# Kernel optimization log

Measured on AMD Instinct MI355X. Metric: run time of the kernel, lower is better.

Reference implementation:

```python
import jax, jax.numpy as jnp
import numpy as np
import math

B, LT, LS, D, H, DFF = 4, 1024, 1024, 1024, 16, 4096
DK = D // H
EPS = 1e-5


def setup_inputs() -> dict:
    key = jax.random.key(0)
    ks = jax.random.split(key, 32)
    n = lambda i, shape, s=0.02: jax.random.normal(ks[i], shape, jnp.float32) * s
    inp = {
        'tgt': jax.random.normal(ks[0], (B, LT, D), jnp.float32),
        'memory': jax.random.normal(ks[1], (B, LS, D), jnp.float32),
        'src_pad_mask': jnp.zeros((B, LT, LS), dtype=bool),
        'tgt_mask': jnp.broadcast_to(jnp.triu(jnp.ones((LT, LT), dtype=bool), 1), (B, LT, LT)),
        # self-attention projections
        'self_wq': n(2, (D, D)), 'self_bq': jnp.zeros((D,)),
        'self_wk': n(3, (D, D)), 'self_bk': jnp.zeros((D,)),
        'self_wv': n(4, (D, D)), 'self_bv': jnp.zeros((D,)),
        'self_wo': n(5, (D, D)), 'self_bo': jnp.zeros((D,)),
        # cross-attention projections
        'cross_wq': n(6, (D, D)), 'cross_bq': jnp.zeros((D,)),
        'cross_wk': n(7, (D, D)), 'cross_bk': jnp.zeros((D,)),
        'cross_wv': n(8, (D, D)), 'cross_bv': jnp.zeros((D,)),
        'cross_wo': n(9, (D, D)), 'cross_bo': jnp.zeros((D,)),
        # layer norms (pre-norm)
        'ln1_g': jnp.ones((D,)), 'ln1_b': jnp.zeros((D,)),
        'ln2_g': jnp.ones((D,)), 'ln2_b': jnp.zeros((D,)),
        'ln3_g': jnp.ones((D,)), 'ln3_b': jnp.zeros((D,)),
        # feed forward
        'ffn_w1': n(10, (D, DFF)), 'ffn_b1': jnp.zeros((DFF,)),
        'ffn_w2': n(11, (DFF, D)), 'ffn_b2': jnp.zeros((D,)),
    }
    return inp


def _layernorm(x, g, b):
    mu = jnp.mean(x, axis=-1, keepdims=True)
    var = jnp.mean(jnp.square(x - mu), axis=-1, keepdims=True)
    return (x - mu) * jax.lax.rsqrt(var + EPS) * g + b


def _mha(xq, xkv, wq, bq, wk, bk, wv, bv, wo, bo, mask):
    b, lq, d = xq.shape
    lk = xkv.shape[1]
    q = (xq @ wq + bq).reshape(b, lq, H, DK).transpose(0, 2, 1, 3) / math.sqrt(DK)
    k = (xkv @ wk + bk).reshape(b, lk, H, DK).transpose(0, 2, 1, 3)
    v = (xkv @ wv + bv).reshape(b, lk, H, DK).transpose(0, 2, 1, 3)
    scores = jnp.einsum('bhqd,bhkd->bhqk', q, k)  # [B,H,Lq,Lk]
    scores = jnp.where(mask[:, None], -1e18, scores)
    attn = jax.nn.softmax(scores, axis=-1)  # dropout p=0 (eval)
    ctx = jnp.einsum('bhqk,bhkd->bhqd', attn, v)
    ctx = ctx.transpose(0, 2, 1, 3).reshape(b, lq, d)
    return ctx @ wo + bo


def reference(tgt, memory, src_pad_mask, tgt_mask,
              self_wq, self_bq, self_wk, self_bk, self_wv, self_bv, self_wo, self_bo,
              cross_wq, cross_bq, cross_wk, cross_bk, cross_wv, cross_bv, cross_wo, cross_bo,
              ln1_g, ln1_b, ln2_g, ln2_b, ln3_g, ln3_b,
              ffn_w1, ffn_b1, ffn_w2, ffn_b2):
    # pre-norm sublayer 1: self attention
    x = tgt + _mha(_layernorm(tgt, ln1_g, ln1_b), _layernorm(tgt, ln1_g, ln1_b),
                   self_wq, self_bq, self_wk, self_bk, self_wv, self_bv, self_wo, self_bo, tgt_mask)
    # pre-norm sublayer 2: cross attention
    x = x + _mha(_layernorm(x, ln2_g, ln2_b), memory,
                 cross_wq, cross_bq, cross_wk, cross_bk, cross_wv, cross_bv, cross_wo, cross_bo, src_pad_mask)
    # pre-norm sublayer 3: FFN
    h = _layernorm(x, ln3_g, ln3_b)
    x = x + (jax.nn.gelu(h @ ffn_w1 + ffn_b1) @ ffn_w2 + ffn_b2)
    return x
```

## Files before the change

kernel.cpp:

```cpp
#include <hip/hip_runtime.h>

typedef unsigned short u16;
typedef __attribute__((ext_vector_type(8))) __bf16 bf16x8;
typedef __attribute__((ext_vector_type(4))) float floatx4;

__device__ inline float bf2f(u16 u) {
    union { unsigned int i; float f; } x; x.i = ((unsigned int)u) << 16; return x.f;
}
__device__ inline u16 f2bf(float f) {
    __bf16 h = (__bf16)f; return __builtin_bit_cast(unsigned short, h);
}
__device__ inline float load_f(u16 v) { return bf2f(v); }
__device__ inline float load_f(float v) { return v; }

__device__ inline floatx4 mfma_bf16(bf16x8 a, bf16x8 b, floatx4 c) {
    return __builtin_amdgcn_mfma_f32_16x16x32_bf16(a, b, c, 0, 0, 0);
}

__device__ inline float gelu_tanh(float x) {
    float u = 0.7978845608028654f * (x + 0.044715f * x * x * x);
    u = fminf(fmaxf(u, -15.f), 15.f);
    float e = __expf(2.f * u);
    float th = (e - 1.f) / (e + 1.f);
    return 0.5f * x * (1.f + th);
}

__device__ inline void async16(const void* g, void* l) {
    __builtin_amdgcn_global_load_lds(
        (const __attribute__((address_space(1))) unsigned int*)g,
        (__attribute__((address_space(3))) unsigned int*)l, 16, 0, 0);
}

__global__ __launch_bounds__(256)
void detect_dtype(const u16* __restrict__ p, int* __restrict__ flag) {
    int t = threadIdx.x, cnt = 0;
    #pragma unroll
    for (int j = 0; j < 8; ++j) {
        unsigned e = (p[t * 8 + j] >> 7) & 0xFF;
        cnt += (e >= 100 && e <= 140) ? 1 : 0;
    }
    __shared__ int s[256];
    s[t] = cnt; __syncthreads();
    for (int off = 128; off; off >>= 1) { if (t < off) s[t] += s[t + off]; __syncthreads(); }
    if (t == 0) *flag = (s[0] < 1844) ? 1 : 0;
}

__global__ __launch_bounds__(256)
void convert_to_bf16(const void* __restrict__ src, u16* __restrict__ dst, int n,
                     const int* __restrict__ flag) {
    int f = *flag;
    int i = (blockIdx.x * 256 + threadIdx.x) * 4;
    if (i < n) {
        #pragma unroll
        for (int j = 0; j < 4; ++j)
            dst[i + j] = f ? f2bf(((const float*)src)[i + j]) : ((const u16*)src)[i + j];
    }
}

__global__ __launch_bounds__(256)
void convert_tgt(const void* __restrict__ src, u16* __restrict__ dst,
                 float* __restrict__ X, int n, const int* __restrict__ flag) {
    int f = *flag;
    int i = (blockIdx.x * 256 + threadIdx.x) * 4;
    if (i < n) {
        #pragma unroll
        for (int j = 0; j < 4; ++j) {
            float v; u16 hv;
            if (f) { v = ((const float*)src)[i + j]; hv = f2bf(v); }
            else   { hv = ((const u16*)src)[i + j]; v = bf2f(hv); }
            dst[i + j] = hv;
            X[i + j] = v;
        }
    }
}

struct VecTab { const void* src[16]; int n[16]; int off[16]; };
__global__ __launch_bounds__(256)
void convert_vecs(VecTab tab, u16* __restrict__ dst, const int* __restrict__ flag) {
    int f = *flag;
    int b = blockIdx.x;
    const void* s = tab.src[b];
    int n = tab.n[b];
    u16* d = dst + tab.off[b];
    for (int i = threadIdx.x; i < n; i += 256)
        d[i] = f ? f2bf(((const float*)s)[i]) : ((const u16*)s)[i];
}

__global__ __launch_bounds__(256)
void store_out(const float* __restrict__ X, void* __restrict__ out, int n,
               const int* __restrict__ flag) {
    int f = *flag;
    int i = (blockIdx.x * 256 + threadIdx.x) * 4;
    if (i < n) {
        #pragma unroll
        for (int j = 0; j < 4; ++j) {
            float v = X[i + j];
            if (f) ((float*)out)[i + j] = v;
            else   ((u16*)out)[i + j] = f2bf(v);
        }
    }
}

__global__ __launch_bounds__(256)
void transpose_any(const void* __restrict__ src, u16* __restrict__ dst, int R, int C,
                   const int* __restrict__ flag) {
    int f = *flag;
    __shared__ u16 tile[32][33];
    int tx = threadIdx.x & 31, ty = threadIdx.x >> 5;
    int r0 = blockIdx.y * 32, c0 = blockIdx.x * 32;
    #pragma unroll
    for (int i = 0; i < 32; i += 8) {
        size_t idx = (size_t)(r0 + ty + i) * C + c0 + tx;
        tile[ty + i][tx] = f ? f2bf(((const float*)src)[idx]) : ((const u16*)src)[idx];
    }
    __syncthreads();
    #pragma unroll
    for (int i = 0; i < 32; i += 8)
        dst[(size_t)(c0 + ty + i) * R + r0 + tx] = tile[tx][ty + i];
}

template <typename TIN>
__global__ __launch_bounds__(256)
void lnorm(const TIN* __restrict__ Xin, const u16* __restrict__ gg,
           const u16* __restrict__ bb, u16* __restrict__ Y) {
    const int row = blockIdx.x, t = threadIdx.x;
    const TIN* xr = Xin + (size_t)row * 1024;
    float x[4]; float s1 = 0.f, s2 = 0.f;
    #pragma unroll
    for (int i = 0; i < 4; ++i) {
        float v = load_f(xr[i * 256 + t]);
        x[i] = v; s1 += v; s2 += v * v;
    }
    #pragma unroll
    for (int m = 1; m < 64; m <<= 1) { s1 += __shfl_xor(s1, m, 64); s2 += __shfl_xor(s2, m, 64); }
    __shared__ float red[8];
    if ((t & 63) == 0) { red[(t >> 6) * 2] = s1; red[(t >> 6) * 2 + 1] = s2; }
    __syncthreads();
    s1 = red[0] + red[2] + red[4] + red[6];
    s2 = red[1] + red[3] + red[5] + red[7];
    float mu = s1 * (1.f / 1024.f);
    float var = s2 * (1.f / 1024.f) - mu * mu;
    float rs = rsqrtf(var + 1e-5f);
    #pragma unroll
    for (int i = 0; i < 4; ++i) {
        int idx = i * 256 + t;
        float yv = (x[i] - mu) * rs * bf2f(gg[idx]) + bf2f(bb[idx]);
        Y[(size_t)row * 1024 + idx] = f2bf(yv);
    }
}

__global__ __launch_bounds__(256, 2)
void gemm_bt2(const u16* __restrict__ A, const u16* __restrict__ Bt,
              const u16* __restrict__ bias, u16* __restrict__ C,
              float* __restrict__ Xres, int M, int N, int K, int ldc, int epi) {
    __shared__ alignas(16) u16 As[128 * 32];
    __shared__ alignas(16) u16 Bs[128 * 32];
    const int t = threadIdx.x;
    const int lane = t & 63, w = t >> 6;
    const int l15 = lane & 15, quad = lane >> 4;
    const int m0 = blockIdx.y * 128, n0 = blockIdx.x * 128;
    const int wm = (w >> 1) * 64, wn = (w & 1) * 64;
    const int ksl = K / gridDim.z;
    const int kb = blockIdx.z * ksl, ke = kb + ksl;
    const int srow = lane >> 2, scol = (lane & 3) * 8;
    const u16* ga = A + (size_t)(m0 + w * 32 + srow) * K + scol;
    const u16* gb = Bt + (size_t)(n0 + w * 32 + srow) * K + scol;
    u16* lA0 = &As[(w * 32) * 32];
    u16* lA1 = &As[(w * 32 + 16) * 32];
    u16* lB0 = &Bs[(w * 32) * 32];
    u16* lB1 = &Bs[(w * 32 + 16) * 32];
    floatx4 acc[4][4] = {};

    for (int k0 = kb; k0 < ke; k0 += 32) {
        __syncthreads();
        async16(ga + k0, lA0);
        async16(ga + (size_t)16 * K + k0, lA1);
        async16(gb + k0, lB0);
        async16(gb + (size_t)16 * K + k0, lB1);
        __syncthreads();
        bf16x8 af[4], bfr[4];
        #pragma unroll
        for (int i = 0; i < 4; ++i) {
            af[i]  = *(const bf16x8*)&As[(wm + i * 16 + l15) * 32 + quad * 8];
            bfr[i] = *(const bf16x8*)&Bs[(wn + i * 16 + l15) * 32 + quad * 8];
        }
        #pragma unroll
        for (int mi = 0; mi < 4; ++mi)
            #pragma unroll
            for (int ni = 0; ni < 4; ++ni)
                acc[mi][ni] = mfma_bf16(af[mi], bfr[ni], acc[mi][ni]);
    }

    const bool addb = (blockIdx.z == 0);
    #pragma unroll
    for (int mi = 0; mi < 4; ++mi) {
        #pragma unroll
        for (int ni = 0; ni < 4; ++ni) {
            int gn = n0 + wn + ni * 16 + l15;
            float bv = addb ? bf2f(bias[gn]) : 0.f;
            #pragma unroll
            for (int r = 0; r < 4; ++r) {
                int gm = m0 + wm + mi * 16 + quad * 4 + r;
                float v = acc[mi][ni][r] + bv;
                size_t idx = (size_t)gm * ldc + gn;
                if (epi == 0)      C[idx] = f2bf(v);
                else if (epi == 1) C[idx] = f2bf(gelu_tanh(v));
                else               atomicAdd(&Xres[idx], v);
            }
        }
    }
}

#define SCL2 0.18033688011112042f
__global__ __launch_bounds__(256, 2)
void attn_fwd2(const u16* __restrict__ QKV, u16* __restrict__ CTX, int causal) {
    __shared__ alignas(16) u16 Ks[64 * 72];
    __shared__ alignas(16) u16 Vst[64 * 72];
    __shared__ alignas(16) u16 Sw[4][16 * 72];
    const int t = threadIdx.x;
    const int lane = t & 63, w = t >> 6;
    const int l15 = lane & 15, quad = lane >> 4;
    const int q0 = blockIdx.x * 64, h = blockIdx.y, b = blockIdx.z;
    const int qrow = q0 + w * 16 + l15;
    const u16* qp = QKV + (size_t)(b * 1024 + qrow) * 3072 + h * 64;
    bf16x8 aq0 = *(const bf16x8*)(qp + quad * 8);
    bf16x8 aq1 = *(const bf16x8*)(qp + 32 + quad * 8);
    floatx4 O[4] = {};
    float mo[4], lo[4];
    #pragma unroll
    for (int r = 0; r < 4; ++r) { mo[r] = -1e30f; lo[r] = 0.f; }

    const int skey = t >> 2, snn = t & 3, sd0 = (t & 3) * 16;
    const int swz = skey ^ (snn << 3);
    const int kend = causal ? (q0 + 64) : 1024;
    for (int kt = 0; kt < kend; kt += 64) {
        __syncthreads();
        {
            const u16* kvb = QKV + (size_t)(b * 1024 + kt + skey) * 3072 + h * 64 + sd0;
            bf16x8 k0v = *(const bf16x8*)(kvb + 1024);
            bf16x8 k1v = *(const bf16x8*)(kvb + 1024 + 8);
            *(bf16x8*)&Ks[skey * 72 + sd0] = k0v;
            *(bf16x8*)&Ks[skey * 72 + sd0 + 8] = k1v;
            bf16x8 v0v = *(const bf16x8*)(kvb + 2048);
            bf16x8 v1v = *(const bf16x8*)(kvb + 2048 + 8);
            #pragma unroll
            for (int j = 0; j < 8; ++j) Vst[(sd0 + j) * 72 + swz] = ((u16*)&v0v)[j];
            #pragma unroll
            for (int j = 0; j < 8; ++j) Vst[(sd0 + 8 + j) * 72 + swz] = ((u16*)&v1v)[j];
        }
        __syncthreads();
        floatx4 S[4];
        #pragma unroll
        for (int kg = 0; kg < 4; ++kg) {
            bf16x8 bk0 = *(const bf16x8*)&Ks[(kg * 16 + l15) * 72 + quad * 8];
            bf16x8 bk1 = *(const bf16x8*)&Ks[(kg * 16 + l15) * 72 + 32 + quad * 8];
            floatx4 z = {};
            z = mfma_bf16(aq0, bk0, z);
            z = mfma_bf16(aq1, bk1, z);
            S[kg] = z;
        }
        const bool domask = causal && (kt == q0);
        float al[4];
        #pragma unroll
        for (int r = 0; r < 4; ++r) {
            #pragma unroll
            for (int kg = 0; kg < 4; ++kg) {
                float s = S[kg][r] * SCL2;
                if (domask) {
                    int kg_glob = kt + kg * 16 + l15;
                    int qg = q0 + w * 16 + quad * 4 + r;
                    if (kg_glob > qg) s = -1e30f;
                }
                S[kg][r] = s;
            }
            float v = fmaxf(fmaxf(S[0][r], S[1][r]), fmaxf(S[2][r], S[3][r]));
            #pragma unroll
            for (int msk = 1; msk < 16; msk <<= 1) v = fmaxf(v, __shfl_xor(v, msk, 64));
            float mn = fmaxf(mo[r], v);
            al[r] = exp2f(mo[r] - mn);
            float ssum = 0.f;
            #pragma unroll
            for (int kg = 0; kg < 4; ++kg) {
                float p = exp2f(S[kg][r] - mn);
                S[kg][r] = p; ssum += p;
            }
            #pragma unroll
            for (int msk = 1; msk < 16; msk <<= 1) ssum += __shfl_xor(ssum, msk, 64);
            lo[r] = lo[r] * al[r] + ssum;
            mo[r] = mn;
        }
        #pragma unroll
        for (int kg = 0; kg < 4; ++kg)
            #pragma unroll
            for (int r = 0; r < 4; ++r)
                Sw[w][(quad * 4 + r) * 72 + kg * 16 + l15] = f2bf(S[kg][r]);
        #pragma unroll
        for (int g = 0; g < 4; ++g)
            #pragma unroll
            for (int r = 0; r < 4; ++r)
                O[g][r] *= al[r];
        bf16x8 ap0 = *(const bf16x8*)&Sw[w][l15 * 72 + quad * 8];
        bf16x8 ap1 = *(const bf16x8*)&Sw[w][l15 * 72 + 32 + quad * 8];
        #pragma unroll
        for (int g = 0; g < 4; ++g) {
            bf16x8 bv0 = *(const bf16x8*)&Vst[(g * 16 + l15) * 72 + ((quad ^ g) << 3)];
            bf16x8 bv1 = *(const bf16x8*)&Vst[(g * 16 + l15) * 72 + 32 + ((quad ^ g) << 3)];
            O[g] = mfma_bf16(ap0, bv0, O[g]);
            O[g] = mfma_bf16(ap1, bv1, O[g]);
        }
    }
    #pragma unroll
    for (int r = 0; r < 4; ++r) {
        float inv = 1.0f / lo[r];
        int qg = q0 + w * 16 + quad * 4 + r;
        #pragma unroll
        for (int g = 0; g < 4; ++g)
            CTX[(size_t)(b * 1024 + qg) * 1024 + h * 64 + g * 16 + l15] = f2bf(O[g][r] * inv);
    }
}

extern "C" void kernel_launch(void* const* d_in, const int* in_sizes, int n_in,
                              void* d_out, int out_size, void* d_ws, size_t ws_size,
                              hipStream_t stream) {
    const void* tgt_raw    = d_in[0];
    const void* memory_raw = d_in[1];

    char* ws = (char*)d_ws;
    const size_t MiB = 1024 * 1024;
    float* X   = (float*)ws;
    u16* Y     = (u16*)(ws + 16 * MiB);
    u16* QKV   = (u16*)(ws + 24 * MiB);
    u16* CTX   = (u16*)(ws + 48 * MiB);
    u16* H1    = (u16*)(ws + 24 * MiB);
    u16* wt    = (u16*)(ws + 56 * MiB);
    u16* wqkv_s = wt;
    u16* wo_s  = wt + 3 * 1048576;
    u16* wq_c  = wt + 4 * 1048576;
    u16* wkv_c = wt + 5 * 1048576;
    u16* wo_c  = wt + 7 * 1048576;
    u16* w1t   = wt + 8 * 1048576;
    u16* w2t   = wt + 12 * 1048576;
    u16* tgt_c = (u16*)(ws + 88 * MiB);
    u16* mem_c = (u16*)(ws + 96 * MiB);
    u16* vecs  = (u16*)(ws + 104 * MiB);
    int* flag  = (int*)(ws + 105 * MiB);

    dim3 blk(256);
    detect_dtype<<<1, blk, 0, stream>>>((const u16*)tgt_raw, flag);
    convert_tgt<<<4096, blk, 0, stream>>>(tgt_raw, tgt_c, X, 4096 * 1024, flag);
    convert_to_bf16<<<4096, blk, 0, stream>>>(memory_raw, mem_c, 4096 * 1024, flag);

    VecTab tab;
    const int srcIdx[16] = {5, 7, 9, 11, 13, 15, 17, 19, 20, 21, 22, 23, 24, 25, 27, 29};
    const int offs[16]   = {0, 1024, 2048, 3072, 4096, 5120, 6144, 7168,
                            8192, 9216, 10240, 11264, 12288, 13312, 14336, 18432};
    for (int i = 0; i < 16; ++i) {
        tab.src[i] = d_in[srcIdx[i]];
        tab.n[i] = (i == 14) ? 4096 : 1024;
        tab.off[i] = offs[i];
    }
    convert_vecs<<<16, blk, 0, stream>>>(tab, vecs, flag);
    u16* b_qkv_s = vecs;            u16* b_o_s  = vecs + 3072;
    u16* b_q_c   = vecs + 4096;     u16* b_kv_c = vecs + 5120;
    u16* b_o_c   = vecs + 7168;
    u16* g1 = vecs + 8192;  u16* be1 = vecs + 9216;
    u16* g2 = vecs + 10240; u16* be2 = vecs + 11264;
    u16* g3 = vecs + 12288; u16* be3 = vecs + 13312;
    u16* b_ff1 = vecs + 14336; u16* b_ff2 = vecs + 18432;

    dim3 tg32(32, 32);
    transpose_any<<<tg32, blk, 0, stream>>>(d_in[4],  wqkv_s,               1024, 1024, flag);
    transpose_any<<<tg32, blk, 0, stream>>>(d_in[6],  wqkv_s + 1048576,     1024, 1024, flag);
    transpose_any<<<tg32, blk, 0, stream>>>(d_in[8],  wqkv_s + 2 * 1048576, 1024, 1024, flag);
    transpose_any<<<tg32, blk, 0, stream>>>(d_in[10], wo_s,                 1024, 1024, flag);
    transpose_any<<<tg32, blk, 0, stream>>>(d_in[12], wq_c,                 1024, 1024, flag);
    transpose_any<<<tg32, blk, 0, stream>>>(d_in[14], wkv_c,                1024, 1024, flag);
    transpose_any<<<tg32, blk, 0, stream>>>(d_in[16], wkv_c + 1048576,      1024, 1024, flag);
    transpose_any<<<tg32, blk, 0, stream>>>(d_in[18], wo_c,                 1024, 1024, flag);
    transpose_any<<<dim3(128, 32), blk, 0, stream>>>(d_in[26], w1t, 1024, 4096, flag);
    transpose_any<<<dim3(32, 128), blk, 0, stream>>>(d_in[28], w2t, 4096, 1024, flag);

    const int NTOK = 4096;
    dim3 g1k(8, 32), g2k(16, 32), g3k(24, 32), g4k(32, 32);
    dim3 g1k_s2(8, 32, 2);
    dim3 g1k_s4(8, 32, 4);
    dim3 ga(16, 16, 4);

    lnorm<u16><<<4096, blk, 0, stream>>>(tgt_c, g1, be1, Y);
    gemm_bt2<<<g3k, blk, 0, stream>>>(Y, wqkv_s, b_qkv_s, QKV, nullptr, NTOK, 3072, 1024, 3072, 0);
    attn_fwd2<<<ga, blk, 0, stream>>>(QKV, CTX, 1);
    gemm_bt2<<<g1k_s2, blk, 0, stream>>>(CTX, wo_s, b_o_s, nullptr, X, NTOK, 1024, 1024, 1024, 2);

    lnorm<float><<<4096, blk, 0, stream>>>(X, g2, be2, Y);
    gemm_bt2<<<g1k, blk, 0, stream>>>(Y, wq_c, b_q_c, QKV, nullptr, NTOK, 1024, 1024, 3072, 0);
    gemm_bt2<<<g2k, blk, 0, stream>>>(mem_c, wkv_c, b_kv_c, QKV + 1024, nullptr, NTOK, 2048, 1024, 3072, 0);
    attn_fwd2<<<ga, blk, 0, stream>>>(QKV, CTX, 0);
    gemm_bt2<<<g1k_s2, blk, 0, stream>>>(CTX, wo_c, b_o_c, nullptr, X, NTOK, 1024, 1024, 1024, 2);

    lnorm<float><<<4096, blk, 0, stream>>>(X, g3, be3, Y);
    gemm_bt2<<<g4k, blk, 0, stream>>>(Y, w1t, b_ff1, H1, nullptr, NTOK, 4096, 1024, 4096, 1);
    gemm_bt2<<<g1k_s4, blk, 0, stream>>>(H1, w2t, b_ff2, nullptr, X, NTOK, 1024, 4096, 1024, 2);

    store_out<<<4096, blk, 0, stream>>>(X, d_out, NTOK * 1024, flag);
}
```

Baseline: 738.9 us.

## Batch transposes and conversions, template GEMM tile height, drop split-K atomics

Merges the ten weight transposes into one table-driven launch and the two input conversions into one kernel, which cuts launch overhead. Templates the GEMM on M-tile height and uses 64-row tiles without split-K for the N=1024 GEMMs, so the residual add becomes a plain read-modify-write instead of atomics. FFN2 keeps a 2-way split with atomics. Occupancy hints rise to 4 blocks per CU for GEMM and attention, which may raise register pressure or cause spills.

```diff
diff --git a/kernel.cpp b/kernel.cpp
--- a/kernel.cpp
+++ b/kernel.cpp
@@ -46,31 +46,22 @@
 }
 
 __global__ __launch_bounds__(256)
-void convert_to_bf16(const void* __restrict__ src, u16* __restrict__ dst, int n,
-                     const int* __restrict__ flag) {
+void convert_big(const void* __restrict__ tgt, const void* __restrict__ mem,
+                 u16* __restrict__ tgt_c, u16* __restrict__ mem_c,
+                 float* __restrict__ X, const int* __restrict__ flag) {
     int f = *flag;
-    int i = (blockIdx.x * 256 + threadIdx.x) * 4;
-    if (i < n) {
-        #pragma unroll
-        for (int j = 0; j < 4; ++j)
-            dst[i + j] = f ? f2bf(((const float*)src)[i + j]) : ((const u16*)src)[i + j];
-    }
-}
-
-__global__ __launch_bounds__(256)
-void convert_tgt(const void* __restrict__ src, u16* __restrict__ dst,
-                 float* __restrict__ X, int n, const int* __restrict__ flag) {
-    int f = *flag;
-    int i = (blockIdx.x * 256 + threadIdx.x) * 4;
-    if (i < n) {
-        #pragma unroll
-        for (int j = 0; j < 4; ++j) {
-            float v; u16 hv;
-            if (f) { v = ((const float*)src)[i + j]; hv = f2bf(v); }
-            else   { hv = ((const u16*)src)[i + j]; v = bf2f(hv); }
-            dst[i + j] = hv;
-            X[i + j] = v;
-        }
+    int b = blockIdx.x;
+    bool isT = b < 4096;
+    const void* s = isT ? tgt : mem;
+    u16* d = isT ? tgt_c : mem_c;
+    int i = (((isT ? b : b - 4096) * 256) + threadIdx.x) * 4;
+    #pragma unroll
+    for (int j = 0; j < 4; ++j) {
+        float v; u16 hv;
+        if (f) { v = ((const float*)s)[i + j]; hv = f2bf(v); }
+        else   { hv = ((const u16*)s)[i + j]; v = bf2f(hv); }
+        d[i + j] = hv;
+        if (isT) X[i + j] = v;
     }
 }
 
@@ -101,13 +92,27 @@
     }
 }
 
-__global__ __launch_bounds__(256)
-void transpose_any(const void* __restrict__ src, u16* __restrict__ dst, int R, int C,
-                   const int* __restrict__ flag) {
+struct TransTab {
+    const void* src[10]; u16* dst[10];
+    int C[10]; int start[10];
+};
+__global__ __launch_bounds__(256)
+void transpose_batch(TransTab tb, const int* __restrict__ flag) {
     int f = *flag;
+    int bid = blockIdx.x;
+    int seg = 0;
+    #pragma unroll
+    for (int i = 1; i < 10; ++i) if (bid >= tb.start[i]) seg = i;
+    int local = bid - tb.start[seg];
+    const void* src = tb.src[seg];
+    u16* dst = tb.dst[seg];
+    int C = tb.C[seg];
+    int ct = C >> 5;
+    int by = local / ct, bx = local - by * ct;
+    int R = (seg < 8) ? 1024 : ((seg == 8) ? 1024 : 4096);
     __shared__ u16 tile[32][33];
     int tx = threadIdx.x & 31, ty = threadIdx.x >> 5;
-    int r0 = blockIdx.y * 32, c0 = blockIdx.x * 32;
+    int r0 = by * 32, c0 = bx * 32;
     #pragma unroll
     for (int i = 0; i < 32; i += 8) {
         size_t idx = (size_t)(r0 + ty + i) * C + c0 + tx;
@@ -149,43 +154,47 @@
     }
 }
 
-__global__ __launch_bounds__(256, 2)
+template <int TM>
+__global__ __launch_bounds__(256, 4)
 void gemm_bt2(const u16* __restrict__ A, const u16* __restrict__ Bt,
               const u16* __restrict__ bias, u16* __restrict__ C,
               float* __restrict__ Xres, int M, int N, int K, int ldc, int epi) {
-    __shared__ alignas(16) u16 As[128 * 32];
+    __shared__ alignas(16) u16 As[TM * 32];
     __shared__ alignas(16) u16 Bs[128 * 32];
+    constexpr int MI = TM / 32;
+    constexpr int AROWS = TM / 4;
     const int t = threadIdx.x;
     const int lane = t & 63, w = t >> 6;
     const int l15 = lane & 15, quad = lane >> 4;
-    const int m0 = blockIdx.y * 128, n0 = blockIdx.x * 128;
-    const int wm = (w >> 1) * 64, wn = (w & 1) * 64;
+    const int m0 = blockIdx.y * TM, n0 = blockIdx.x * 128;
+    const int wm = (w >> 1) * (TM / 2), wn = (w & 1) * 64;
     const int ksl = K / gridDim.z;
     const int kb = blockIdx.z * ksl, ke = kb + ksl;
     const int srow = lane >> 2, scol = (lane & 3) * 8;
-    const u16* ga = A + (size_t)(m0 + w * 32 + srow) * K + scol;
+    const u16* ga = A + (size_t)(m0 + w * AROWS + srow) * K + scol;
     const u16* gb = Bt + (size_t)(n0 + w * 32 + srow) * K + scol;
-    u16* lA0 = &As[(w * 32) * 32];
-    u16* lA1 = &As[(w * 32 + 16) * 32];
+    u16* lA = &As[(w * AROWS) * 32];
     u16* lB0 = &Bs[(w * 32) * 32];
     u16* lB1 = &Bs[(w * 32 + 16) * 32];
-    floatx4 acc[4][4] = {};
+    floatx4 acc[MI][4] = {};
 
     for (int k0 = kb; k0 < ke; k0 += 32) {
         __syncthreads();
-        async16(ga + k0, lA0);
-        async16(ga + (size_t)16 * K + k0, lA1);
+        #pragma unroll
+        for (int c = 0; c < TM / 64; ++c)
+            async16(ga + (size_t)(c * 16) * K + k0, lA + c * 16 * 32);
         async16(gb + k0, lB0);
         async16(gb + (size_t)16 * K + k0, lB1);
         __syncthreads();
-        bf16x8 af[4], bfr[4];
-        #pragma unroll
-        for (int i = 0; i < 4; ++i) {
-            af[i]  = *(const bf16x8*)&As[(wm + i * 16 + l15) * 32 + quad * 8];
+        bf16x8 af[MI], bfr[4];
+        #pragma unroll
+        for (int i = 0; i < MI; ++i)
+            af[i] = *(const bf16x8*)&As[(wm + i * 16 + l15) * 32 + quad * 8];
+        #pragma unroll
+        for (int i = 0; i < 4; ++i)
             bfr[i] = *(const bf16x8*)&Bs[(wn + i * 16 + l15) * 32 + quad * 8];
-        }
-        #pragma unroll
-        for (int mi = 0; mi < 4; ++mi)
+        #pragma unroll
+        for (int mi = 0; mi < MI; ++mi)
             #pragma unroll
             for (int ni = 0; ni < 4; ++ni)
                 acc[mi][ni] = mfma_bf16(af[mi], bfr[ni], acc[mi][ni]);
@@ -193,7 +202,7 @@
 
     const bool addb = (blockIdx.z == 0);
     #pragma unroll
-    for (int mi = 0; mi < 4; ++mi) {
+    for (int mi = 0; mi < MI; ++mi) {
         #pragma unroll
         for (int ni = 0; ni < 4; ++ni) {
             int gn = n0 + wn + ni * 16 + l15;
@@ -205,6 +214,7 @@
                 size_t idx = (size_t)gm * ldc + gn;
                 if (epi == 0)      C[idx] = f2bf(v);
                 else if (epi == 1) C[idx] = f2bf(gelu_tanh(v));
+                else if (epi == 2) Xres[idx] += v;
                 else               atomicAdd(&Xres[idx], v);
             }
         }
@@ -212,7 +222,7 @@
 }
 
 #define SCL2 0.18033688011112042f
-__global__ __launch_bounds__(256, 2)
+__global__ __launch_bounds__(256, 4)
 void attn_fwd2(const u16* __restrict__ QKV, u16* __restrict__ CTX, int causal) {
     __shared__ alignas(16) u16 Ks[64 * 72];
     __shared__ alignas(16) u16 Vst[64 * 72];
@@ -347,8 +357,7 @@
 
     dim3 blk(256);
     detect_dtype<<<1, blk, 0, stream>>>((const u16*)tgt_raw, flag);
-    convert_tgt<<<4096, blk, 0, stream>>>(tgt_raw, tgt_c, X, 4096 * 1024, flag);
-    convert_to_bf16<<<4096, blk, 0, stream>>>(memory_raw, mem_c, 4096 * 1024, flag);
+    convert_big<<<8192, blk, 0, stream>>>(tgt_raw, memory_raw, tgt_c, mem_c, X, flag);
 
     VecTab tab;
     const int srcIdx[16] = {5, 7, 9, 11, 13, 15, 17, 19, 20, 21, 22, 23, 24, 25, 27, 29};
@@ -368,38 +377,41 @@
     u16* g3 = vecs + 12288; u16* be3 = vecs + 13312;
     u16* b_ff1 = vecs + 14336; u16* b_ff2 = vecs + 18432;
 
-    dim3 tg32(32, 32);
-    transpose_any<<<tg32, blk, 0, stream>>>(d_in[4],  wqkv_s,               1024, 1024, flag);
-    transpose_any<<<tg32, blk, 0, stream>>>(d_in[6],  wqkv_s + 1048576,     1024, 1024, flag);
-    transpose_any<<<tg32, blk, 0, stream>>>(d_in[8],  wqkv_s + 2 * 1048576, 1024, 1024, flag);
-    transpose_any<<<tg32, blk, 0, stream>>>(d_in[10], wo_s,                 1024, 1024, flag);
-    transpose_any<<<tg32, blk, 0, stream>>>(d_in[12], wq_c,                 1024, 1024, flag);
-    transpose_any<<<tg32, blk, 0, stream>>>(d_in[14], wkv_c,                1024, 1024, flag);
-    transpose_any<<<tg32, blk, 0, stream>>>(d_in[16], wkv_c + 1048576,      1024, 1024, flag);
-    transpose_any<<<tg32, blk, 0, stream>>>(d_in[18], wo_c,                 1024, 1024, flag);
-    transpose_any<<<dim3(128, 32), blk, 0, stream>>>(d_in[26], w1t, 1024, 4096, flag);
-    transpose_any<<<dim3(32, 128), blk, 0, stream>>>(d_in[28], w2t, 4096, 1024, flag);
+    TransTab tt;
+    const void* tsrc[10] = {d_in[4], d_in[6], d_in[8], d_in[10], d_in[12],
+                            d_in[14], d_in[16], d_in[18], d_in[26], d_in[28]};
+    u16* tdst[10] = {wqkv_s, wqkv_s + 1048576, wqkv_s + 2 * 1048576, wo_s, wq_c,
+                     wkv_c, wkv_c + 1048576, wo_c, w1t, w2t};
+    int start = 0;
+    for (int i = 0; i < 10; ++i) {
+        tt.src[i] = tsrc[i]; tt.dst[i] = tdst[i];
+        tt.C[i] = (i == 8) ? 4096 : 1024;
+        tt.start[i] = start;
+        int R = (i == 9) ? 4096 : 1024;
+        start += (R / 32) * (tt.C[i] / 32);
+    }
+    transpose_batch<<<start, blk, 0, stream>>>(tt, flag);
 
     const int NTOK = 4096;
-    dim3 g1k(8, 32), g2k(16, 32), g3k(24, 32), g4k(32, 32);
-    dim3 g1k_s2(8, 32, 2);
-    dim3 g1k_s4(8, 32, 4);
+    dim3 gQKV(24, 32), gKV(16, 32), gFF1(32, 32);
+    dim3 gN1k(8, 64);
+    dim3 gFF2(8, 64, 2);
     dim3 ga(16, 16, 4);
 
     lnorm<u16><<<4096, blk, 0, stream>>>(tgt_c, g1, be1, Y);
-    gemm_bt2<<<g3k, blk, 0, stream>>>(Y, wqkv_s, b_qkv_s, QKV, nullptr, NTOK, 3072, 1024, 3072, 0);
+    gemm_bt2<128><<<gQKV, blk, 0, stream>>>(Y, wqkv_s, b_qkv_s, QKV, nullptr, NTOK, 3072, 1024, 3072, 0);
     attn_fwd2<<<ga, blk, 0, stream>>>(QKV, CTX, 1);
-    gemm_bt2<<<g1k_s2, blk, 0, stream>>>(CTX, wo_s, b_o_s, nullptr, X, NTOK, 1024, 1024, 1024, 2);
+    gemm_bt2<64><<<gN1k, blk, 0, stream>>>(CTX, wo_s, b_o_s, nullptr, X, NTOK, 1024, 1024, 1024, 2);
 
     lnorm<float><<<4096, blk, 0, stream>>>(X, g2, be2, Y);
-    gemm_bt2<<<g1k, blk, 0, stream>>>(Y, wq_c, b_q_c, QKV, nullptr, NTOK, 1024, 1024, 3072, 0);
-    gemm_bt2<<<g2k, blk, 0, stream>>>(mem_c, wkv_c, b_kv_c, QKV + 1024, nullptr, NTOK, 2048, 1024, 3072, 0);
+    gemm_bt2<64><<<gN1k, blk, 0, stream>>>(Y, wq_c, b_q_c, QKV, nullptr, NTOK, 1024, 1024, 3072, 0);
+    gemm_bt2<128><<<gKV, blk, 0, stream>>>(mem_c, wkv_c, b_kv_c, QKV + 1024, nullptr, NTOK, 2048, 1024, 3072, 0);
     attn_fwd2<<<ga, blk, 0, stream>>>(QKV, CTX, 0);
-    gemm_bt2<<<g1k_s2, blk, 0, stream>>>(CTX, wo_c, b_o_c, nullptr, X, NTOK, 1024, 1024, 1024, 2);
+    gemm_bt2<64><<<gN1k, blk, 0, stream>>>(CTX, wo_c, b_o_c, nullptr, X, NTOK, 1024, 1024, 1024, 2);
 
     lnorm<float><<<4096, blk, 0, stream>>>(X, g3, be3, Y);
-    gemm_bt2<<<g4k, blk, 0, stream>>>(Y, w1t, b_ff1, H1, nullptr, NTOK, 4096, 1024, 4096, 1);
-    gemm_bt2<<<g1k_s4, blk, 0, stream>>>(H1, w2t, b_ff2, nullptr, X, NTOK, 1024, 4096, 1024, 2);
+    gemm_bt2<128><<<gFF1, blk, 0, stream>>>(Y, w1t, b_ff1, H1, nullptr, NTOK, 4096, 1024, 4096, 1);
+    gemm_bt2<64><<<gFF2, blk, 0, stream>>>(H1, w2t, b_ff2, nullptr, X, NTOK, 1024, 4096, 1024, 3);
 
     store_out<<<4096, blk, 0, stream>>>(X, d_out, NTOK * 1024, flag);
 }
```

After: 672.3 us. 9.0% less time.
